# Performance work log

Measured on AMD Instinct MI355X. Metric: run time of the kernel, lower is better.

## Reference

```python
import jax, jax.numpy as jnp
import numpy as np

EPS = 1e-5
H = 8  # num_heads

def ln(x, g, b):
    m = x.mean(-1, keepdims=True)
    v = ((x - m) ** 2).mean(-1, keepdims=True)
    return (x - m) / jnp.sqrt(v + EPS) * g + b

def gca(qf, kf, p):
    # Gated cross-modal attention (eval mode, dropout off, mask all-True => no mask)
    (nqg, nqb, nkg, nkb, wq, bq, wk, bk, wv, bv, wo, bo,
     wgp, bgp, g1w, g1b, glng, glnb, g2w, g2b) = p
    B, Sq, _ = qf.shape
    Sk = kf.shape[1]
    E = wq.shape[1]
    D = E // H
    qn = ln(qf, nqg, nqb)
    kn = ln(kf, nkg, nkb)
    q = (qn @ wq + bq).reshape(B, Sq, H, D)
    k = (kn @ wk + bk).reshape(B, Sk, H, D)
    v = (kn @ wv + bv).reshape(B, Sk, H, D)
    scores = jnp.einsum('bqhd,bkhd->bhqk', q, k) * (D ** -0.5)
    w = jax.nn.softmax(scores, axis=-1)          # [B,H,Sq,Sk]
    ctx = jnp.einsum('bhqk,bkhd->bqhd', w, v).reshape(B, Sq, E)
    att = ctx @ wo + bo                          # cross-attention output
    qp = qf @ wgp + bgp                          # query projected for gating
    h = jnp.concatenate([qp, att], axis=-1) @ g1w + g1b
    gate = jax.nn.sigmoid(jax.nn.gelu(ln(h, glng, glnb), approximate=False) @ g2w + g2b)
    return qp + gate * att, w

def ff(x, lng, lnb, w1, b1, w2, b2):
    y = jax.nn.gelu(ln(x, lng, lnb) @ w1 + b1, approximate=False)
    return x + (y @ w2 + b2)

def setup_inputs() -> dict:
    B, Sv, St, Vd, Td, F = 8, 1024, 512, 1024, 768, 512
    keys = iter(jax.random.split(jax.random.key(0), 80))
    def nrm(shape):
        return jax.random.normal(next(keys), shape, jnp.float32) * 0.02
    d = {}
    d['vision_features'] = jax.random.normal(next(keys), (B, Sv, Vd), jnp.float32)
    d['text_features'] = jax.random.normal(next(keys), (B, St, Td), jnp.float32)
    def attn_params(pfx, qd, kd, e):
        d[pfx + 'nq_g'] = jnp.ones(qd); d[pfx + 'nq_b'] = jnp.zeros(qd)
        d[pfx + 'nk_g'] = jnp.ones(kd); d[pfx + 'nk_b'] = jnp.zeros(kd)
        d[pfx + 'wq'] = nrm((qd, e)); d[pfx + 'bq'] = jnp.zeros(e)
        d[pfx + 'wk'] = nrm((kd, e)); d[pfx + 'bk'] = jnp.zeros(e)
        d[pfx + 'wv'] = nrm((kd, e)); d[pfx + 'bv'] = jnp.zeros(e)
        d[pfx + 'wo'] = nrm((e, e)); d[pfx + 'bo'] = jnp.zeros(e)
        d[pfx + 'wgp'] = nrm((qd, e)); d[pfx + 'bgp'] = jnp.zeros(e)
        d[pfx + 'g1w'] = nrm((2 * e, e)); d[pfx + 'g1b'] = jnp.zeros(e)
        d[pfx + 'glng'] = jnp.ones(e); d[pfx + 'glnb'] = jnp.zeros(e)
        d[pfx + 'g2w'] = nrm((e, e)); d[pfx + 'g2b'] = jnp.zeros(e)
    attn_params('t2v_', Td, Vd, F)  # text queries attend to vision
    attn_params('v2t_', Vd, Td, F)  # vision queries attend to text
    for pfx in ('vff_', 'tff_'):
        d[pfx + 'lng'] = jnp.ones(F); d[pfx + 'lnb'] = jnp.zeros(F)
        d[pfx + 'w1'] = nrm((F, 4 * F)); d[pfx + 'b1'] = jnp.zeros(4 * F)
        d[pfx + 'w2'] = nrm((4 * F, F)); d[pfx + 'b2'] = jnp.zeros(F)
    return d

def reference(vision_features, text_features,
              t2v_nq_g, t2v_nq_b, t2v_nk_g, t2v_nk_b, t2v_wq, t2v_bq, t2v_wk, t2v_bk, t2v_wv, t2v_bv, t2v_wo, t2v_bo, t2v_wgp, t2v_bgp, t2v_g1w, t2v_g1b, t2v_glng, t2v_glnb, t2v_g2w, t2v_g2b,
              v2t_nq_g, v2t_nq_b, v2t_nk_g, v2t_nk_b, v2t_wq, v2t_bq, v2t_wk, v2t_bk, v2t_wv, v2t_bv, v2t_wo, v2t_bo, v2t_wgp, v2t_bgp, v2t_g1w, v2t_g1b, v2t_glng, v2t_glnb, v2t_g2w, v2t_g2b,
              vff_lng, vff_lnb, vff_w1, vff_b1, vff_w2, vff_b2,
              tff_lng, tff_lnb, tff_w1, tff_b1, tff_w2, tff_b2):
    t2v_p = (t2v_nq_g, t2v_nq_b, t2v_nk_g, t2v_nk_b, t2v_wq, t2v_bq, t2v_wk, t2v_bk, t2v_wv, t2v_bv, t2v_wo, t2v_bo, t2v_wgp, t2v_bgp, t2v_g1w, t2v_g1b, t2v_glng, t2v_glnb, t2v_g2w, t2v_g2b)
    v2t_p = (v2t_nq_g, v2t_nq_b, v2t_nk_g, v2t_nk_b, v2t_wq, v2t_bq, v2t_wk, v2t_bk, v2t_wv, v2t_bv, v2t_wo, v2t_bo, v2t_wgp, v2t_bgp, v2t_g1w, v2t_g1b, v2t_glng, v2t_glnb, v2t_g2w, v2t_g2b)
    text_att, t2v_w = gca(text_features, vision_features, t2v_p)
    vis_att, v2t_w = gca(vision_features, text_features, v2t_p)
    vision_out = ff(vis_att, vff_lng, vff_lnb, vff_w1, vff_b1, vff_w2, vff_b2)
    text_out = ff(text_att, tff_lng, tff_lnb, tff_w1, tff_b1, tff_w2, tff_b2)
    return (vision_out, text_out, t2v_w, v2t_w)
```

## Files before the change

kernel.cpp:

```cpp
#include <hip/hip_runtime.h>
#include <math.h>


typedef __attribute__((ext_vector_type(8))) short s16x8;
typedef __attribute__((ext_vector_type(4))) float f32x4;
typedef __attribute__((ext_vector_type(4))) unsigned short us4;

__device__ __forceinline__ float gelu_exact(float x) {
  return 0.5f * x * (1.0f + erff(x * 0.70710678118654752f));
}
__device__ __forceinline__ float sigmoidf_(float x) {
  return 1.0f / (1.0f + expf(-x));
}
__device__ __forceinline__ unsigned short f2bf(float f) {
  unsigned int u = __float_as_uint(f);
  u += 0x7fffu + ((u >> 16) & 1u);
  return (unsigned short)(u >> 16);
}

template <bool GELU>
__global__ __launch_bounds__(256) void ln_kernel(
    const float* __restrict__ x, const float* __restrict__ g,
    const float* __restrict__ b, unsigned short* __restrict__ out, int cols) {
  const int row = blockIdx.x;
  const float2* xr = (const float2*)(x + (size_t)row * cols);
  const float2* g2 = (const float2*)g;
  const float2* b2 = (const float2*)b;
  const int n2 = cols >> 1;
  const int tid = threadIdx.x;
  float s = 0.f, ss = 0.f;
  for (int c = tid; c < n2; c += 256) {
    float2 v = xr[c];
    s += v.x + v.y;
    ss += v.x * v.x + v.y * v.y;
  }
#pragma unroll
  for (int off = 32; off; off >>= 1) {
    s += __shfl_down(s, off, 64);
    ss += __shfl_down(ss, off, 64);
  }
  __shared__ float rs[4], rss[4], stat[2];
  const int lane = tid & 63, wid = tid >> 6;
  if (lane == 0) {
    rs[wid] = s;
    rss[wid] = ss;
  }
  __syncthreads();
  if (tid == 0) {
    float ts = rs[0] + rs[1] + rs[2] + rs[3];
    float tss = rss[0] + rss[1] + rss[2] + rss[3];
    float m = ts / (float)cols;
    float var = tss / (float)cols - m * m;
    stat[0] = m;
    stat[1] = 1.0f / sqrtf(var + 1e-5f);
  }
  __syncthreads();
  const float m = stat[0], inv = stat[1];
  ushort2* o2 = (ushort2*)(out + (size_t)row * cols);
  for (int c = tid; c < n2; c += 256) {
    float2 v = xr[c];
    float2 gg = g2[c], bb = b2[c];
    float o0 = (v.x - m) * inv * gg.x + bb.x;
    float o1 = (v.y - m) * inv * gg.y + bb.y;
    if (GELU) {
      o0 = gelu_exact(o0);
      o1 = gelu_exact(o1);
    }
    ushort2 r;
    r.x = f2bf(o0);
    r.y = f2bf(o1);
    o2[c] = r;
  }
}

__global__ __launch_bounds__(256) void cast_kernel(
    const float* __restrict__ x, unsigned short* __restrict__ o, int n4) {
  const int stride = gridDim.x * 256;
  for (int i = blockIdx.x * 256 + threadIdx.x; i < n4; i += stride) {
    float4 v = ((const float4*)x)[i];
    us4 r = {f2bf(v.x), f2bf(v.y), f2bf(v.z), f2bf(v.w)};
    ((us4*)o)[i] = r;
  }
}

struct TP {
  const float* s[8];
  unsigned short* d[8];
};
__global__ __launch_bounds__(256) void tc_kernel(TP tp, int R, int C) {
  __shared__ unsigned short tile[32][33];
  const float* src = tp.s[blockIdx.z];
  unsigned short* dst = tp.d[blockIdx.z];
  const int r0 = blockIdx.y * 32, c0 = blockIdx.x * 32;
  const int t = threadIdx.x;
  const int tr = t >> 3, tc4 = (t & 7) * 4;
  float4 v = *(const float4*)(src + (size_t)(r0 + tr) * C + c0 + tc4);
  tile[tr][tc4 + 0] = f2bf(v.x);
  tile[tr][tc4 + 1] = f2bf(v.y);
  tile[tr][tc4 + 2] = f2bf(v.z);
  tile[tr][tc4 + 3] = f2bf(v.w);
  __syncthreads();
  us4 o = {tile[tc4 + 0][tr], tile[tc4 + 1][tr], tile[tc4 + 2][tr],
           tile[tc4 + 3][tr]};
  *(us4*)(dst + (size_t)(c0 + tr) * R + r0 + tc4) = o;
}

template <int SK>
__global__ __launch_bounds__(256) void attn_sm(
    const unsigned short* __restrict__ qp, const unsigned short* __restrict__ kp,
    float* __restrict__ w, unsigned short* __restrict__ wb, int Sq,
    float scale) {
  constexpr int TPW = SK / 64;
  const int z = blockIdx.y, b = z >> 3, h = z & 7;
  const int q0 = blockIdx.x * 16;
  const int t = threadIdx.x, wv = t >> 6, lane = t & 63;
  const int hh = lane >> 4, r16 = lane & 15;
  const unsigned short* qrow =
      qp + (size_t)(b * Sq + q0 + r16) * 512 + h * 64 + 4 * hh;
  s16x8 aq[2];
#pragma unroll
  for (int kt = 0; kt < 2; ++kt) {
    ((unsigned long long*)&aq[kt])[0] =
        *(const unsigned long long*)(qrow + kt * 32);
    ((unsigned long long*)&aq[kt])[1] =
        *(const unsigned long long*)(qrow + kt * 32 + 16);
  }
  const unsigned short* kbase = kp + (size_t)b * SK * 512 + h * 64 + 4 * hh;
  f32x4 sc[TPW];
#pragma unroll
  for (int tl = 0; tl < TPW; ++tl) {
    const unsigned short* krow =
        kbase + (size_t)(wv * (TPW * 16) + tl * 16 + r16) * 512;
    s16x8 b0, b1;
    ((unsigned long long*)&b0)[0] = *(const unsigned long long*)(krow);
    ((unsigned long long*)&b0)[1] = *(const unsigned long long*)(krow + 16);
    ((unsigned long long*)&b1)[0] = *(const unsigned long long*)(krow + 32);
    ((unsigned long long*)&b1)[1] = *(const unsigned long long*)(krow + 48);
    f32x4 a = {};
    a = __builtin_amdgcn_mfma_f32_16x16x32_bf16(aq[0], b0, a, 0, 0, 0);
    a = __builtin_amdgcn_mfma_f32_16x16x32_bf16(aq[1], b1, a, 0, 0, 0);
    sc[tl] = a * scale;
  }
  __shared__ float redM[4][16], redS[4][16];
  float mx[4], sm[4];
#pragma unroll
  for (int q = 0; q < 4; ++q) {
    float m = sc[0][q];
#pragma unroll
    for (int tl = 1; tl < TPW; ++tl) m = fmaxf(m, sc[tl][q]);
    mx[q] = m;
  }
#pragma unroll
  for (int off = 1; off < 16; off <<= 1)
#pragma unroll
    for (int q = 0; q < 4; ++q)
      mx[q] = fmaxf(mx[q], __shfl_xor(mx[q], off, 64));
  if (r16 == 0) {
#pragma unroll
    for (int q = 0; q < 4; ++q) redM[wv][hh * 4 + q] = mx[q];
  }
  __syncthreads();
#pragma unroll
  for (int q = 0; q < 4; ++q) {
    const int rr = hh * 4 + q;
    mx[q] = fmaxf(fmaxf(redM[0][rr], redM[1][rr]),
                  fmaxf(redM[2][rr], redM[3][rr]));
    sm[q] = 0.f;
  }
#pragma unroll
  for (int tl = 0; tl < TPW; ++tl)
#pragma unroll
    for (int q = 0; q < 4; ++q) {
      const float e = expf(sc[tl][q] - mx[q]);
      sc[tl][q] = e;
      sm[q] += e;
    }
#pragma unroll
  for (int off = 1; off < 16; off <<= 1)
#pragma unroll
    for (int q = 0; q < 4; ++q) sm[q] += __shfl_xor(sm[q], off, 64);
  if (r16 == 0) {
#pragma unroll
    for (int q = 0; q < 4; ++q) redS[wv][hh * 4 + q] = sm[q];
  }
  __syncthreads();
  float inv[4];
#pragma unroll
  for (int q = 0; q < 4; ++q) {
    const int rr = hh * 4 + q;
    inv[q] = 1.0f / (redS[0][rr] + redS[1][rr] + redS[2][rr] + redS[3][rr]);
  }
  float* wrow = w + ((size_t)z * Sq + q0) * SK;
  unsigned short* wbrow = wb + ((size_t)z * Sq + q0) * SK;
#pragma unroll
  for (int tl = 0; tl < TPW; ++tl) {
    const int col = wv * (TPW * 16) + tl * 16 + r16;
#pragma unroll
    for (int q = 0; q < 4; ++q) {
      const float v = sc[tl][q] * inv[q];
      const size_t o = (size_t)(hh * 4 + q) * SK + col;
      wrow[o] = v;
      wbrow[o] = f2bf(v);
    }
  }
}

enum { EPI_B = 0, EPI_BG = 1, EPI_BR = 2, EPI_BGATE = 3, EPI_SC = 4, EPI_KV = 5 };

template <int ROWS>
__device__ __forceinline__ void stage_tile(unsigned short (*lds)[40],
                                           const unsigned short* __restrict__ g,
                                           size_t ld) {
  const int t = threadIdx.x;
  const int jr = t & 3;
  const int B0 = (jr < 2) ? (jr * 32) : ((jr - 2) * 32 + 8);
#pragma unroll
  for (int p = 0; p < ROWS / 64; ++p) {
    const int row = (t >> 2) + p * 64;
    uint4 u = *(const uint4*)(g + (size_t)row * ld + jr * 8);
    char* dst = (char*)(&lds[row][0]) + B0;
    *(unsigned long long*)dst = ((const unsigned long long*)&u)[0];
    *(unsigned long long*)(dst + 16) = ((const unsigned long long*)&u)[1];
  }
}

template <int EPI, int OM, int BN, bool CONCAT>
__global__ __launch_bounds__(256) void mm(
    const unsigned short* __restrict__ A0,
    const unsigned short* __restrict__ A1, int lda0, int lda1, int K0, int K,
    const unsigned short* __restrict__ Bt, int ldb,
    const float* __restrict__ bias, const float* __restrict__ bias2,
    const float* __restrict__ X1, const float* __restrict__ X2,
    float* __restrict__ outF, unsigned short* __restrict__ outB,
    unsigned short* __restrict__ outT, int ldc, int skShift, float scale,
    size_t aZb, size_t aZh, size_t bZb, size_t bZh, size_t cZb, size_t cZh) {
  constexpr int WN = BN / 2;
  constexpr int NJ = WN / 16;
  __shared__ unsigned short As[128][40];
  __shared__ unsigned short Bs[BN][40];
  const int z = blockIdx.z;
  const size_t zb = z >> 3, zh = z & 7;
  const int m0 = blockIdx.y * 128, n0 = blockIdx.x * BN;
  const int t = threadIdx.x;
  const int w = t >> 6, lane = t & 63;
  const int h = lane >> 4, r16 = lane & 15;
  const int wm = w >> 1, wn = w & 1;
  const unsigned short* Ab = A0 + zb * aZb + zh * aZh + (size_t)m0 * lda0;
  const unsigned short* A1b = CONCAT ? (A1 + (size_t)m0 * lda1) : nullptr;
  const unsigned short* Bb = Bt + zb * bZb + zh * bZh + (size_t)n0 * ldb;
  f32x4 acc[4][NJ] = {};
  for (int k0 = 0; k0 < K; k0 += 32) {
    const unsigned short* ag;
    size_t lda;
    if (CONCAT && k0 >= K0) {
      ag = A1b + (k0 - K0);
      lda = (size_t)lda1;
    } else {
      ag = Ab + k0;
      lda = (size_t)lda0;
    }
    stage_tile<128>(As, ag, lda);
    stage_tile<BN>(Bs, Bb + k0, (size_t)ldb);
    __syncthreads();
    const unsigned short* ap = &As[wm * 64 + r16][h * 8];
    const unsigned short* bp = &Bs[wn * WN + r16][h * 8];
    s16x8 av[4], bv[NJ];
#pragma unroll
    for (int i = 0; i < 4; ++i) av[i] = *(const s16x8*)(ap + i * 640);
#pragma unroll
    for (int j = 0; j < NJ; ++j) bv[j] = *(const s16x8*)(bp + j * 640);
#pragma unroll
    for (int i = 0; i < 4; ++i)
#pragma unroll
      for (int j = 0; j < NJ; ++j)
        acc[i][j] = __builtin_amdgcn_mfma_f32_16x16x32_bf16(av[i], bv[j],
                                                            acc[i][j], 0, 0, 0);
    __syncthreads();
  }
  const size_t cz = zb * cZb + zh * cZh;
#pragma unroll
  for (int i = 0; i < 4; ++i) {
    const int rr = m0 + wm * 64 + i * 16 + h * 4;
#pragma unroll
    for (int j = 0; j < NJ; ++j) {
      const int cc = n0 + wn * WN + j * 16 + r16;
      if (EPI == EPI_KV) {
        const bool isK = (cc < 512);
        const float bb = isK ? bias[cc] : bias2[cc - 512];
#pragma unroll
        for (int q = 0; q < 4; ++q) {
          const float v = acc[i][j][q] + bb;
          const int r = rr + q;
          if (isK) {
            outB[(size_t)r * 512 + cc] = f2bf(v);
          } else {
            const int b_ = r >> skShift;
            const int sk = r - (b_ << skShift);
            outT[(((size_t)b_ * 512 + (cc - 512)) << skShift) + sk] = f2bf(v);
          }
        }
      } else {
        const float bb = (EPI == EPI_SC) ? 0.f : bias[cc];
#pragma unroll
        for (int q = 0; q < 4; ++q) {
          float v = acc[i][j][q];
          v = (EPI == EPI_SC) ? v * scale : v + bb;
          if (EPI == EPI_BG) v = gelu_exact(v);
          const size_t idx = cz + (size_t)(rr + q) * ldc + cc;
          if (EPI == EPI_BR) v = X1[idx] + v;
          if (EPI == EPI_BGATE) v = X1[idx] + sigmoidf_(v) * X2[idx];
          if (OM & 1) outF[idx] = v;
          if (OM & 2) outB[idx] = f2bf(v);
        }
      }
    }
  }
}

extern "C" void kernel_launch(void* const* d_in, const int* in_sizes, int n_in,
                              void* d_out, int out_size, void* d_ws,
                              size_t ws_size, hipStream_t stream) {
  (void)in_sizes;
  (void)n_in;
  (void)out_size;
  (void)ws_size;
  const int B = 8, Sv = 1024, St = 512, Vd = 1024, Td = 768, E = 512;
  auto inf = [&](int i) { return (const float*)d_in[i]; };
  float* out = (float*)d_out;
  char* ws = (char*)d_ws;
  float* out_vis = out;
  float* out_txt = out + 4194304;
  float* w_t2v = out + 6291456;
  float* w_v2t = out + 39845888;

  const size_t W0 = 0;
  const size_t R1o = 67108864;
  const size_t R2o = 83886080;
  const size_t R3o = 100663296;
  const size_t R4o = 109051904;
  const size_t R5o = 117440512;
  const size_t R6o = 125829120;
  auto U = [&](size_t o) { return (unsigned short*)(ws + o); };
  auto F = [&](size_t o) { return (float*)(ws + o); };

  {
    const int pb = 2;
    const int Sq = St, Sk = Sv, Mq = B * Sq, Mk = B * Sk;
    unsigned short* wq_t = U(R3o + 0);
    unsigned short* wk_t = U(R3o + 786432);
    unsigned short* wv_t = U(R3o + 1835008);
    unsigned short* wo_t = U(R3o + 2883584);
    unsigned short* wgp_t = U(R3o + 3407872);
    unsigned short* g1w_t = U(R3o + 4194304);
    unsigned short* g2w_t = U(R3o + 5242880);
    {
      TP tp{};
      tp.s[0] = inf(pb + 4); tp.d[0] = wq_t;
      tp.s[1] = inf(pb + 12); tp.d[1] = wgp_t;
      tc_kernel<<<dim3(16, 24, 2), 256, 0, stream>>>(tp, 768, 512);
    }
    {
      TP tp{};
      tp.s[0] = inf(pb + 6); tp.d[0] = wk_t;
      tp.s[1] = inf(pb + 8); tp.d[1] = wv_t;
      tp.s[2] = inf(pb + 14); tp.d[2] = g1w_t;
      tc_kernel<<<dim3(16, 32, 3), 256, 0, stream>>>(tp, 1024, 512);
    }
    {
      TP tp{};
      tp.s[0] = inf(pb + 10); tp.d[0] = wo_t;
      tp.s[1] = inf(pb + 18); tp.d[1] = g2w_t;
      tc_kernel<<<dim3(16, 16, 2), 256, 0, stream>>>(tp, 512, 512);
    }
    unsigned short* qn = U(W0);
    unsigned short* kn = U(R1o);
    unsigned short* q_bf = U(R5o);
    unsigned short* k_bf = U(R6o);
    unsigned short* vt = U(R4o);
    unsigned short* w_bf = U(W0);
    unsigned short* ctx_bf = U(R1o);
    float* att_f = F(R2o);
    unsigned short* att_bf = U(W0 + 50331648);
    unsigned short* txt_bf = U(W0);
    float* qp_f = F(R1o + 8388608);
    unsigned short* qp_bf = U(W0 + 58720256);
    float* h_f = F(W0 + 16777216);
    unsigned short* hg = U(W0);

    ln_kernel<false><<<Mq, 256, 0, stream>>>(inf(1), inf(pb + 0), inf(pb + 1),
                                             qn, Td);
    ln_kernel<false><<<Mk, 256, 0, stream>>>(inf(0), inf(pb + 2), inf(pb + 3),
                                             kn, Vd);
    mm<EPI_B, 2, 64, false><<<dim3(8, 32), 256, 0, stream>>>(
        qn, nullptr, Td, 0, Td, Td, wq_t, Td, inf(pb + 5), nullptr, nullptr,
        nullptr, nullptr, q_bf, nullptr, E, 0, 1.f, 0, 0, 0, 0, 0, 0);
    mm<EPI_KV, 0, 128, false><<<dim3(8, 64), 256, 0, stream>>>(
        kn, nullptr, Vd, 0, Vd, Vd, wk_t, Vd, inf(pb + 7), inf(pb + 9),
        nullptr, nullptr, nullptr, k_bf, vt, 0, 10, 1.f, 0, 0, 0, 0, 0, 0);
    attn_sm<1024><<<dim3(Sq / 16, 64), 256, 0, stream>>>(q_bf, k_bf, w_t2v,
                                                         w_bf, Sq, 0.125f);
    mm<EPI_SC, 2, 64, false><<<dim3(1, Sq / 128, 64), 256, 0, stream>>>(
        w_bf, nullptr, Sk, 0, Sk, Sk, vt, Sk, nullptr, nullptr, nullptr,
        nullptr, nullptr, ctx_bf, nullptr, E, 0, 1.f, (size_t)8 * Sq * Sk,
        (size_t)Sq * Sk, (size_t)E * Sk, (size_t)64 * Sk, (size_t)Sq * E, 64);
    mm<EPI_B, 3, 64, false><<<dim3(8, 32), 256, 0, stream>>>(
        ctx_bf, nullptr, E, 0, E, E, wo_t, E, inf(pb + 11), nullptr, nullptr,
        nullptr, att_f, att_bf, nullptr, E, 0, 1.f, 0, 0, 0, 0, 0, 0);
    cast_kernel<<<1024, 256, 0, stream>>>(inf(1), txt_bf, Mq * Td / 4);
    mm<EPI_B, 3, 64, false><<<dim3(8, 32), 256, 0, stream>>>(
        txt_bf, nullptr, Td, 0, Td, Td, wgp_t, Td, inf(pb + 13), nullptr,
        nullptr, nullptr, qp_f, qp_bf, nullptr, E, 0, 1.f, 0, 0, 0, 0, 0, 0);
    mm<EPI_B, 1, 64, true><<<dim3(8, 32), 256, 0, stream>>>(
        qp_bf, att_bf, E, E, E, 2 * E, g1w_t, 2 * E, inf(pb + 15), nullptr,
        nullptr, nullptr, h_f, nullptr, nullptr, E, 0, 1.f, 0, 0, 0, 0, 0, 0);
    ln_kernel<true><<<Mq, 256, 0, stream>>>(h_f, inf(pb + 16), inf(pb + 17),
                                            hg, E);
    mm<EPI_BGATE, 1, 64, false><<<dim3(8, 32), 256, 0, stream>>>(
        hg, nullptr, E, 0, E, E, g2w_t, E, inf(pb + 19), nullptr, qp_f, att_f,
        out_txt, nullptr, nullptr, E, 0, 1.f, 0, 0, 0, 0, 0, 0);
  }
  {
    const int pb = 22;
    const int Sq = Sv, Sk = St, Mq = B * Sq, Mk = B * St;
    unsigned short* wq_t = U(R3o + 0);
    unsigned short* wk_t = U(R3o + 1048576);
    unsigned short* wv_t = U(R3o + 1835008);
    unsigned short* wo_t = U(R3o + 2621440);
    unsigned short* wgp_t = U(R3o + 3145728);
    unsigned short* g1w_t = U(R3o + 4194304);
    unsigned short* g2w_t = U(R3o + 5242880);
    {
      TP tp{};
      tp.s[0] = inf(pb + 4); tp.d[0] = wq_t;
      tp.s[1] = inf(pb + 12); tp.d[1] = wgp_t;
      tp.s[2] = inf(pb + 14); tp.d[2] = g1w_t;
      tc_kernel<<<dim3(16, 32, 3), 256, 0, stream>>>(tp, 1024, 512);
    }
    {
      TP tp{};
      tp.s[0] = inf(pb + 6); tp.d[0] = wk_t;
      tp.s[1] = inf(pb + 8); tp.d[1] = wv_t;
      tc_kernel<<<dim3(16, 24, 2), 256, 0, stream>>>(tp, 768, 512);
    }
    {
      TP tp{};
      tp.s[0] = inf(pb + 10); tp.d[0] = wo_t;
      tp.s[1] = inf(pb + 18); tp.d[1] = g2w_t;
      tc_kernel<<<dim3(16, 16, 2), 256, 0, stream>>>(tp, 512, 512);
    }
    unsigned short* qn = U(W0);
    unsigned short* kn = U(R1o);
    unsigned short* q_bf = U(R5o);
    unsigned short* k_bf = U(R6o);
    unsigned short* vt = U(R4o);
    unsigned short* w_bf = U(W0);
    unsigned short* ctx_bf = U(R1o);
    float* att_f = F(R2o);
    unsigned short* att_bf = U(W0 + 50331648);
    unsigned short* vis_bf = U(W0);
    float* qp_f = F(R1o);
    unsigned short* qp_bf = U(W0 + 58720256);
    float* h_f = F(W0 + 16777216);
    unsigned short* hg = U(W0);

    ln_kernel<false><<<Mq, 256, 0, stream>>>(inf(0), inf(pb + 0), inf(pb + 1),
                                             qn, Vd);
    ln_kernel<false><<<Mk, 256, 0, stream>>>(inf(1), inf(pb + 2), inf(pb + 3),
                                             kn, Td);
    mm<EPI_B, 2, 128, false><<<dim3(4, 64), 256, 0, stream>>>(
        qn, nullptr, Vd, 0, Vd, Vd, wq_t, Vd, inf(pb + 5), nullptr, nullptr,
        nullptr, nullptr, q_bf, nullptr, E, 0, 1.f, 0, 0, 0, 0, 0, 0);
    mm<EPI_KV, 0, 128, false><<<dim3(8, 32), 256, 0, stream>>>(
        kn, nullptr, Td, 0, Td, Td, wk_t, Td, inf(pb + 7), inf(pb + 9),
        nullptr, nullptr, nullptr, k_bf, vt, 0, 9, 1.f, 0, 0, 0, 0, 0, 0);
    attn_sm<512><<<dim3(Sq / 16, 64), 256, 0, stream>>>(q_bf, k_bf, w_v2t,
                                                        w_bf, Sq, 0.125f);
    mm<EPI_SC, 2, 64, false><<<dim3(1, Sq / 128, 64), 256, 0, stream>>>(
        w_bf, nullptr, Sk, 0, Sk, Sk, vt, Sk, nullptr, nullptr, nullptr,
        nullptr, nullptr, ctx_bf, nullptr, E, 0, 1.f, (size_t)8 * Sq * Sk,
        (size_t)Sq * Sk, (size_t)E * Sk, (size_t)64 * Sk, (size_t)Sq * E, 64);
    mm<EPI_B, 3, 128, false><<<dim3(4, 64), 256, 0, stream>>>(
        ctx_bf, nullptr, E, 0, E, E, wo_t, E, inf(pb + 11), nullptr, nullptr,
        nullptr, att_f, att_bf, nullptr, E, 0, 1.f, 0, 0, 0, 0, 0, 0);
    cast_kernel<<<2048, 256, 0, stream>>>(inf(0), vis_bf, Mq * Vd / 4);
    mm<EPI_B, 3, 128, false><<<dim3(4, 64), 256, 0, stream>>>(
        vis_bf, nullptr, Vd, 0, Vd, Vd, wgp_t, Vd, inf(pb + 13), nullptr,
        nullptr, nullptr, qp_f, qp_bf, nullptr, E, 0, 1.f, 0, 0, 0, 0, 0, 0);
    mm<EPI_B, 1, 128, true><<<dim3(4, 64), 256, 0, stream>>>(
        qp_bf, att_bf, E, E, E, 2 * E, g1w_t, 2 * E, inf(pb + 15), nullptr,
        nullptr, nullptr, h_f, nullptr, nullptr, E, 0, 1.f, 0, 0, 0, 0, 0, 0);
    ln_kernel<true><<<Mq, 256, 0, stream>>>(h_f, inf(pb + 16), inf(pb + 17),
                                            hg, E);
    mm<EPI_BGATE, 1, 128, false><<<dim3(4, 64), 256, 0, stream>>>(
        hg, nullptr, E, 0, E, E, g2w_t, E, inf(pb + 19), nullptr, qp_f, att_f,
        out_vis, nullptr, nullptr, E, 0, 1.f, 0, 0, 0, 0, 0, 0);
  }
  {
    unsigned short* vw1_t = U(R3o + 0);
    unsigned short* vw2_t = U(R3o + 2097152);
    unsigned short* tw1_t = U(R3o + 4194304);
    unsigned short* tw2_t = U(R3o + 6291456);
    {
      TP tp{};
      tp.s[0] = inf(44); tp.d[0] = vw1_t;
      tp.s[1] = inf(50); tp.d[1] = tw1_t;
      tc_kernel<<<dim3(64, 16, 2), 256, 0, stream>>>(tp, 512, 2048);
    }
    {
      TP tp{};
      tp.s[0] = inf(46); tp.d[0] = vw2_t;
      tp.s[1] = inf(52); tp.d[1] = tw2_t;
      tc_kernel<<<dim3(16, 64, 2), 256, 0, stream>>>(tp, 2048, 512);
    }
    unsigned short* lnv = U(W0);
    unsigned short* y_v = U(W0 + 8388608);
    unsigned short* lnt = U(W0 + 41943040);
    unsigned short* y_t = U(W0 + 46137344);
    ln_kernel<false><<<8192, 256, 0, stream>>>(out_vis, inf(42), inf(43), lnv,
                                               512);
    mm<EPI_BG, 2, 128, false><<<dim3(16, 64), 256, 0, stream>>>(
        lnv, nullptr, 512, 0, 512, 512, vw1_t, 512, inf(45), nullptr, nullptr,
        nullptr, nullptr, y_v, nullptr, 2048, 0, 1.f, 0, 0, 0, 0, 0, 0);
    mm<EPI_BR, 1, 128, false><<<dim3(4, 64), 256, 0, stream>>>(
        y_v, nullptr, 2048, 0, 2048, 2048, vw2_t, 2048, inf(47), nullptr,
        out_vis, nullptr, out_vis, nullptr, nullptr, 512, 0, 1.f, 0, 0, 0, 0,
        0, 0);
    ln_kernel<false><<<4096, 256, 0, stream>>>(out_txt, inf(48), inf(49), lnt,
                                               512);
    mm<EPI_BG, 2, 128, false><<<dim3(16, 32), 256, 0, stream>>>(
        lnt, nullptr, 512, 0, 512, 512, tw1_t, 512, inf(51), nullptr, nullptr,
        nullptr, nullptr, y_t, nullptr, 2048, 0, 1.f, 0, 0, 0, 0, 0, 0);
    mm<EPI_BR, 1, 64, false><<<dim3(8, 32), 256, 0, stream>>>(
        y_t, nullptr, 2048, 0, 2048, 2048, tw2_t, 2048, inf(53), nullptr,
        out_txt, nullptr, out_txt, nullptr, nullptr, 512, 0, 1.f, 0, 0, 0, 0,
        0, 0);
  }
}
```

Measured before the change: 1.190 ms.

## Shrink GEMM tiles to 64x64 and double-buffer LDS with register prefetch

The bf16 MFMA GEMM kernel now uses fixed 64x64 output tiles instead of 128xBN. The K-tile loop is restructured to prefetch the next global tile into registers while computing on the current one, using two LDS buffers with a single barrier per iteration. This hides global load latency and increases block count, but each wave does only 4 MFMAs per K step, lowering arithmetic intensity and adding more global/LDS traffic per FLOP.

```diff
diff --git a/kernel.cpp b/kernel.cpp
--- a/kernel.cpp
+++ b/kernel.cpp
@@ -207,24 +207,7 @@
 
 enum { EPI_B = 0, EPI_BG = 1, EPI_BR = 2, EPI_BGATE = 3, EPI_SC = 4, EPI_KV = 5 };
 
-template <int ROWS>
-__device__ __forceinline__ void stage_tile(unsigned short (*lds)[40],
-                                           const unsigned short* __restrict__ g,
-                                           size_t ld) {
-  const int t = threadIdx.x;
-  const int jr = t & 3;
-  const int B0 = (jr < 2) ? (jr * 32) : ((jr - 2) * 32 + 8);
-#pragma unroll
-  for (int p = 0; p < ROWS / 64; ++p) {
-    const int row = (t >> 2) + p * 64;
-    uint4 u = *(const uint4*)(g + (size_t)row * ld + jr * 8);
-    char* dst = (char*)(&lds[row][0]) + B0;
-    *(unsigned long long*)dst = ((const unsigned long long*)&u)[0];
-    *(unsigned long long*)(dst + 16) = ((const unsigned long long*)&u)[1];
-  }
-}
-
-template <int EPI, int OM, int BN, bool CONCAT>
+template <int EPI, int OM, bool CONCAT>
 __global__ __launch_bounds__(256) void mm(
     const unsigned short* __restrict__ A0,
     const unsigned short* __restrict__ A1, int lda0, int lda1, int K0, int K,
@@ -234,56 +217,69 @@
     float* __restrict__ outF, unsigned short* __restrict__ outB,
     unsigned short* __restrict__ outT, int ldc, int skShift, float scale,
     size_t aZb, size_t aZh, size_t bZb, size_t bZh, size_t cZb, size_t cZh) {
-  constexpr int WN = BN / 2;
-  constexpr int NJ = WN / 16;
-  __shared__ unsigned short As[128][40];
-  __shared__ unsigned short Bs[BN][40];
+  __shared__ unsigned short As[2][64][40];
+  __shared__ unsigned short Bs[2][64][40];
   const int z = blockIdx.z;
   const size_t zb = z >> 3, zh = z & 7;
-  const int m0 = blockIdx.y * 128, n0 = blockIdx.x * BN;
+  const int m0 = blockIdx.y * 64, n0 = blockIdx.x * 64;
   const int t = threadIdx.x;
   const int w = t >> 6, lane = t & 63;
   const int h = lane >> 4, r16 = lane & 15;
   const int wm = w >> 1, wn = w & 1;
-  const unsigned short* Ab = A0 + zb * aZb + zh * aZh + (size_t)m0 * lda0;
-  const unsigned short* A1b = CONCAT ? (A1 + (size_t)m0 * lda1) : nullptr;
-  const unsigned short* Bb = Bt + zb * bZb + zh * bZh + (size_t)n0 * ldb;
-  f32x4 acc[4][NJ] = {};
-  for (int k0 = 0; k0 < K; k0 += 32) {
-    const unsigned short* ag;
-    size_t lda;
-    if (CONCAT && k0 >= K0) {
-      ag = A1b + (k0 - K0);
-      lda = (size_t)lda1;
-    } else {
-      ag = Ab + k0;
-      lda = (size_t)lda0;
-    }
-    stage_tile<128>(As, ag, lda);
-    stage_tile<BN>(Bs, Bb + k0, (size_t)ldb);
+  const int sr = t >> 2, jr = t & 3;
+  const int B0 = (jr < 2) ? (jr * 32) : ((jr - 2) * 32 + 8);
+  const unsigned short* Ab =
+      A0 + zb * aZb + zh * aZh + (size_t)(m0 + sr) * lda0 + jr * 8;
+  const unsigned short* A1b =
+      CONCAT ? (A1 + (size_t)(m0 + sr) * lda1 + jr * 8) : nullptr;
+  const unsigned short* Bb =
+      Bt + zb * bZb + zh * bZh + (size_t)(n0 + sr) * ldb + jr * 8;
+  const int NT = K >> 5;
+  auto ldA = [&](int tt) -> uint4 {
+    const int k0 = tt * 32;
+    if (CONCAT && k0 >= K0) return *(const uint4*)(A1b + (k0 - K0));
+    return *(const uint4*)(Ab + k0);
+  };
+  uint4 ua = ldA(0);
+  uint4 ub = *(const uint4*)(Bb);
+  f32x4 acc[2][2] = {};
+  int cur = 0;
+  for (int tt = 0; tt < NT; ++tt) {
+    {
+      char* da = (char*)&As[cur][sr][0] + B0;
+      *(unsigned long long*)da = ((const unsigned long long*)&ua)[0];
+      *(unsigned long long*)(da + 16) = ((const unsigned long long*)&ua)[1];
+      char* db = (char*)&Bs[cur][sr][0] + B0;
+      *(unsigned long long*)db = ((const unsigned long long*)&ub)[0];
+      *(unsigned long long*)(db + 16) = ((const unsigned long long*)&ub)[1];
+    }
+    if (tt + 1 < NT) {
+      ua = ldA(tt + 1);
+      ub = *(const uint4*)(Bb + (tt + 1) * 32);
+    }
     __syncthreads();
-    const unsigned short* ap = &As[wm * 64 + r16][h * 8];
-    const unsigned short* bp = &Bs[wn * WN + r16][h * 8];
-    s16x8 av[4], bv[NJ];
-#pragma unroll
-    for (int i = 0; i < 4; ++i) av[i] = *(const s16x8*)(ap + i * 640);
-#pragma unroll
-    for (int j = 0; j < NJ; ++j) bv[j] = *(const s16x8*)(bp + j * 640);
-#pragma unroll
-    for (int i = 0; i < 4; ++i)
-#pragma unroll
-      for (int j = 0; j < NJ; ++j)
+    s16x8 av[2], bv[2];
+#pragma unroll
+    for (int i = 0; i < 2; ++i)
+      av[i] = *(const s16x8*)&As[cur][wm * 32 + i * 16 + r16][h * 8];
+#pragma unroll
+    for (int j = 0; j < 2; ++j)
+      bv[j] = *(const s16x8*)&Bs[cur][wn * 32 + j * 16 + r16][h * 8];
+#pragma unroll
+    for (int i = 0; i < 2; ++i)
+#pragma unroll
+      for (int j = 0; j < 2; ++j)
         acc[i][j] = __builtin_amdgcn_mfma_f32_16x16x32_bf16(av[i], bv[j],
                                                             acc[i][j], 0, 0, 0);
-    __syncthreads();
+    cur ^= 1;
   }
   const size_t cz = zb * cZb + zh * cZh;
 #pragma unroll
-  for (int i = 0; i < 4; ++i) {
-    const int rr = m0 + wm * 64 + i * 16 + h * 4;
-#pragma unroll
-    for (int j = 0; j < NJ; ++j) {
-      const int cc = n0 + wn * WN + j * 16 + r16;
+  for (int i = 0; i < 2; ++i) {
+    const int rr = m0 + wm * 32 + i * 16 + h * 4;
+#pragma unroll
+    for (int j = 0; j < 2; ++j) {
+      const int cc = n0 + wn * 32 + j * 16 + r16;
       if (EPI == EPI_KV) {
         const bool isK = (cc < 512);
         const float bb = isK ? bias[cc] : bias2[cc - 512];
@@ -391,37 +387,37 @@
                                              qn, Td);
     ln_kernel<false><<<Mk, 256, 0, stream>>>(inf(0), inf(pb + 2), inf(pb + 3),
                                              kn, Vd);
-    mm<EPI_B, 2, 64, false><<<dim3(8, 32), 256, 0, stream>>>(
+    mm<EPI_B, 2, false><<<dim3(8, 64), 256, 0, stream>>>(
         qn, nullptr, Td, 0, Td, Td, wq_t, Td, inf(pb + 5), nullptr, nullptr,
         nullptr, nullptr, q_bf, nullptr, E, 0, 1.f, 0, 0, 0, 0, 0, 0);
-    mm<EPI_KV, 0, 128, false><<<dim3(8, 64), 256, 0, stream>>>(
+    mm<EPI_KV, 0, false><<<dim3(16, 128), 256, 0, stream>>>(
         kn, nullptr, Vd, 0, Vd, Vd, wk_t, Vd, inf(pb + 7), inf(pb + 9),
         nullptr, nullptr, nullptr, k_bf, vt, 0, 10, 1.f, 0, 0, 0, 0, 0, 0);
     attn_sm<1024><<<dim3(Sq / 16, 64), 256, 0, stream>>>(q_bf, k_bf, w_t2v,
                                                          w_bf, Sq, 0.125f);
-    mm<EPI_SC, 2, 64, false><<<dim3(1, Sq / 128, 64), 256, 0, stream>>>(
+    mm<EPI_SC, 2, false><<<dim3(1, Sq / 64, 64), 256, 0, stream>>>(
         w_bf, nullptr, Sk, 0, Sk, Sk, vt, Sk, nullptr, nullptr, nullptr,
         nullptr, nullptr, ctx_bf, nullptr, E, 0, 1.f, (size_t)8 * Sq * Sk,
         (size_t)Sq * Sk, (size_t)E * Sk, (size_t)64 * Sk, (size_t)Sq * E, 64);
-    mm<EPI_B, 3, 64, false><<<dim3(8, 32), 256, 0, stream>>>(
+    mm<EPI_B, 3, false><<<dim3(8, 64), 256, 0, stream>>>(
         ctx_bf, nullptr, E, 0, E, E, wo_t, E, inf(pb + 11), nullptr, nullptr,
         nullptr, att_f, att_bf, nullptr, E, 0, 1.f, 0, 0, 0, 0, 0, 0);
     cast_kernel<<<1024, 256, 0, stream>>>(inf(1), txt_bf, Mq * Td / 4);
-    mm<EPI_B, 3, 64, false><<<dim3(8, 32), 256, 0, stream>>>(
+    mm<EPI_B, 3, false><<<dim3(8, 64), 256, 0, stream>>>(
         txt_bf, nullptr, Td, 0, Td, Td, wgp_t, Td, inf(pb + 13), nullptr,
         nullptr, nullptr, qp_f, qp_bf, nullptr, E, 0, 1.f, 0, 0, 0, 0, 0, 0);
-    mm<EPI_B, 1, 64, true><<<dim3(8, 32), 256, 0, stream>>>(
+    mm<EPI_B, 1, true><<<dim3(8, 64), 256, 0, stream>>>(
         qp_bf, att_bf, E, E, E, 2 * E, g1w_t, 2 * E, inf(pb + 15), nullptr,
         nullptr, nullptr, h_f, nullptr, nullptr, E, 0, 1.f, 0, 0, 0, 0, 0, 0);
     ln_kernel<true><<<Mq, 256, 0, stream>>>(h_f, inf(pb + 16), inf(pb + 17),
                                             hg, E);
-    mm<EPI_BGATE, 1, 64, false><<<dim3(8, 32), 256, 0, stream>>>(
+    mm<EPI_BGATE, 1, false><<<dim3(8, 64), 256, 0, stream>>>(
         hg, nullptr, E, 0, E, E, g2w_t, E, inf(pb + 19), nullptr, qp_f, att_f,
         out_txt, nullptr, nullptr, E, 0, 1.f, 0, 0, 0, 0, 0, 0);
   }
   {
     const int pb = 22;
-    const int Sq = Sv, Sk = St, Mq = B * Sq, Mk = B * St;
+    const int Sq = Sv, Sk = St, Mq = B * Sv, Mk = B * St;
     unsigned short* wq_t = U(R3o + 0);
     unsigned short* wk_t = U(R3o + 1048576);
     unsigned short* wv_t = U(R3o + 1835008);
@@ -467,31 +463,31 @@
                                              qn, Vd);
     ln_kernel<false><<<Mk, 256, 0, stream>>>(inf(1), inf(pb + 2), inf(pb + 3),
                                              kn, Td);
-    mm<EPI_B, 2, 128, false><<<dim3(4, 64), 256, 0, stream>>>(
+    mm<EPI_B, 2, false><<<dim3(8, 128), 256, 0, stream>>>(
         qn, nullptr, Vd, 0, Vd, Vd, wq_t, Vd, inf(pb + 5), nullptr, nullptr,
         nullptr, nullptr, q_bf, nullptr, E, 0, 1.f, 0, 0, 0, 0, 0, 0);
-    mm<EPI_KV, 0, 128, false><<<dim3(8, 32), 256, 0, stream>>>(
+    mm<EPI_KV, 0, false><<<dim3(16, 64), 256, 0, stream>>>(
         kn, nullptr, Td, 0, Td, Td, wk_t, Td, inf(pb + 7), inf(pb + 9),
         nullptr, nullptr, nullptr, k_bf, vt, 0, 9, 1.f, 0, 0, 0, 0, 0, 0);
     attn_sm<512><<<dim3(Sq / 16, 64), 256, 0, stream>>>(q_bf, k_bf, w_v2t,
                                                         w_bf, Sq, 0.125f);
-    mm<EPI_SC, 2, 64, false><<<dim3(1, Sq / 128, 64), 256, 0, stream>>>(
+    mm<EPI_SC, 2, false><<<dim3(1, Sq / 64, 64), 256, 0, stream>>>(
         w_bf, nullptr, Sk, 0, Sk, Sk, vt, Sk, nullptr, nullptr, nullptr,
         nullptr, nullptr, ctx_bf, nullptr, E, 0, 1.f, (size_t)8 * Sq * Sk,
         (size_t)Sq * Sk, (size_t)E * Sk, (size_t)64 * Sk, (size_t)Sq * E, 64);
-    mm<EPI_B, 3, 128, false><<<dim3(4, 64), 256, 0, stream>>>(
+    mm<EPI_B, 3, false><<<dim3(8, 128), 256, 0, stream>>>(
         ctx_bf, nullptr, E, 0, E, E, wo_t, E, inf(pb + 11), nullptr, nullptr,
         nullptr, att_f, att_bf, nullptr, E, 0, 1.f, 0, 0, 0, 0, 0, 0);
     cast_kernel<<<2048, 256, 0, stream>>>(inf(0), vis_bf, Mq * Vd / 4);
-    mm<EPI_B, 3, 128, false><<<dim3(4, 64), 256, 0, stream>>>(
+    mm<EPI_B, 3, false><<<dim3(8, 128), 256, 0, stream>>>(
         vis_bf, nullptr, Vd, 0, Vd, Vd, wgp_t, Vd, inf(pb + 13), nullptr,
         nullptr, nullptr, qp_f, qp_bf, nullptr, E, 0, 1.f, 0, 0, 0, 0, 0, 0);
-    mm<EPI_B, 1, 128, true><<<dim3(4, 64), 256, 0, stream>>>(
+    mm<EPI_B, 1, true><<<dim3(8, 128), 256, 0, stream>>>(
         qp_bf, att_bf, E, E, E, 2 * E, g1w_t, 2 * E, inf(pb + 15), nullptr,
         nullptr, nullptr, h_f, nullptr, nullptr, E, 0, 1.f, 0, 0, 0, 0, 0, 0);
     ln_kernel<true><<<Mq, 256, 0, stream>>>(h_f, inf(pb + 16), inf(pb + 17),
                                             hg, E);
-    mm<EPI_BGATE, 1, 128, false><<<dim3(4, 64), 256, 0, stream>>>(
+    mm<EPI_BGATE, 1, false><<<dim3(8, 128), 256, 0, stream>>>(
         hg, nullptr, E, 0, E, E, g2w_t, E, inf(pb + 19), nullptr, qp_f, att_f,
         out_vis, nullptr, nullptr, E, 0, 1.f, 0, 0, 0, 0, 0, 0);
   }
@@ -518,19 +514,19 @@
     unsigned short* y_t = U(W0 + 46137344);
     ln_kernel<false><<<8192, 256, 0, stream>>>(out_vis, inf(42), inf(43), lnv,
                                                512);
-    mm<EPI_BG, 2, 128, false><<<dim3(16, 64), 256, 0, stream>>>(
+    mm<EPI_BG, 2, false><<<dim3(32, 128), 256, 0, stream>>>(
         lnv, nullptr, 512, 0, 512, 512, vw1_t, 512, inf(45), nullptr, nullptr,
         nullptr, nullptr, y_v, nullptr, 2048, 0, 1.f, 0, 0, 0, 0, 0, 0);
-    mm<EPI_BR, 1, 128, false><<<dim3(4, 64), 256, 0, stream>>>(
+    mm<EPI_BR, 1, false><<<dim3(8, 128), 256, 0, stream>>>(
         y_v, nullptr, 2048, 0, 2048, 2048, vw2_t, 2048, inf(47), nullptr,
         out_vis, nullptr, out_vis, nullptr, nullptr, 512, 0, 1.f, 0, 0, 0, 0,
         0, 0);
     ln_kernel<false><<<4096, 256, 0, stream>>>(out_txt, inf(48), inf(49), lnt,
                                                512);
-    mm<EPI_BG, 2, 128, false><<<dim3(16, 32), 256, 0, stream>>>(
+    mm<EPI_BG, 2, false><<<dim3(32, 64), 256, 0, stream>>>(
         lnt, nullptr, 512, 0, 512, 512, tw1_t, 512, inf(51), nullptr, nullptr,
         nullptr, nullptr, y_t, nullptr, 2048, 0, 1.f, 0, 0, 0, 0, 0, 0);
-    mm<EPI_BR, 1, 64, false><<<dim3(8, 32), 256, 0, stream>>>(
+    mm<EPI_BR, 1, false><<<dim3(8, 64), 256, 0, stream>>>(
         y_t, nullptr, 2048, 0, 2048, 2048, tw2_t, 2048, inf(53), nullptr,
         out_txt, nullptr, out_txt, nullptr, nullptr, 512, 0, 1.f, 0, 0, 0, 0,
         0, 0);
```

After: 1.108 ms. 1.07x faster.
